# Optimization experiments

Measured on AMD Instinct MI355X. Metric: run time of the kernel, lower is better.

The kernel has to match this reference:

```python
import jax, jax.numpy as jnp
import numpy as np

N_ENTITY = 200000
N_RELATIONS = 32
DIM = 64
N_HOP = 2
N_MEMORY = 32
BATCH = 1024
KGE_WEIGHT = 0.01
L2_WEIGHT = 1e-7


def setup_inputs() -> dict:
    key = jax.random.key(0)
    ks = jax.random.split(key, 8)
    items = jax.random.randint(ks[0], (BATCH,), 0, N_ENTITY)
    labels = jax.random.uniform(ks[1], (BATCH,), dtype=jnp.float32)
    memories_h = jax.random.randint(ks[2], (N_HOP, BATCH, N_MEMORY), 0, N_ENTITY)
    memories_r = jax.random.randint(ks[3], (N_HOP, BATCH, N_MEMORY), 0, N_RELATIONS)
    memories_t = jax.random.randint(ks[4], (N_HOP, BATCH, N_MEMORY), 0, N_ENTITY)
    item_table = jax.random.normal(ks[5], (N_ENTITY, DIM), dtype=jnp.float32) * 0.1
    relation_table = jax.random.normal(ks[6], (N_RELATIONS, DIM * DIM), dtype=jnp.float32) * 0.1
    transform_W = jax.random.normal(ks[7], (DIM, DIM), dtype=jnp.float32) * 0.1
    return dict(items=items, labels=labels, memories_h=memories_h,
                memories_r=memories_r, memories_t=memories_t,
                item_table=item_table, relation_table=relation_table,
                transform_W=transform_W)


def _forward(items, labels, memories_h, memories_r, memories_t,
             item_table, relation_table, transform_W):
    v = item_table[items]  # [B, D]
    o_list = []
    kge_loss = jnp.float32(0.0)
    l2_loss = jnp.float32(0.0)
    for hop in range(N_HOP):
        h = item_table[memories_h[hop]]                                   # [B, M, D]
        R = relation_table[memories_r[hop]].reshape(-1, N_MEMORY, DIM, DIM)  # [B, M, D, D]
        t = item_table[memories_t[hop]]                                   # [B, M, D]
        # Rh = R @ h  -> [B, M, D]
        Rh = jnp.einsum('bmij,bmj->bmi', R, h)
        # attention probs over memory slots
        probs = jax.nn.softmax(jnp.einsum('bmi,bi->bm', Rh, v), axis=-1)  # [B, M]
        o = jnp.einsum('bmd,bm->bd', t, probs)                            # [B, D]
        # item_update_mode == 'plus_transform': v = W(v + o)
        v = (v + o) @ transform_W.T
        o_list.append(o)
        # KGE loss: sigmoid(h^T R t), mean over [B, M]
        hRt = jnp.einsum('bmi,bmij,bmj->bm', h, R, t)
        kge_loss = kge_loss + jnp.mean(jax.nn.sigmoid(hRt))
        l2_loss = l2_loss + jnp.sum(h * h) + jnp.sum(t * t) + jnp.sum(R * R)
    kge_loss = -KGE_WEIGHT * kge_loss
    l2_loss = L2_WEIGHT * l2_loss
    # predict with all hops
    y = o_list[-1]
    for i in range(N_HOP - 1):
        y = y + o_list[i]
    scores = jax.nn.sigmoid(jnp.sum(v * y, axis=1))  # [B]
    # BCE loss (torch clamps log at -100)
    logp = jnp.clip(jnp.log(scores), -100.0)
    lognp = jnp.clip(jnp.log(1.0 - scores), -100.0)
    base_loss = -jnp.mean(labels * logp + (1.0 - labels) * lognp)
    loss = base_loss + kge_loss + l2_loss
    return scores, loss, base_loss, kge_loss, l2_loss


def reference(items, labels, memories_h, memories_r, memories_t,
              item_table, relation_table, transform_W):
    return _forward(items, labels, memories_h, memories_r, memories_t,
                    item_table, relation_table, transform_W)
```

## Files before the change

kernel.cpp:

```cpp
#include <hip/hip_runtime.h>
#include <math.h>

#define N_ENTITY 200000
#define N_REL 32
#define DIM 64
#define N_HOP 2
#define N_MEM 32
#define BATCH 1024
#define PAIR_PER_HOP (BATCH * N_MEM)
#define N_PAIR (N_HOP * PAIR_PER_HOP)
#define CAP 3072
#define JBLK 32
#define WPB 4
#define NBLK_PAIRS (JBLK * N_REL * WPB)
#define TPAD 68

typedef __attribute__((ext_vector_type(8))) short short8;
typedef __attribute__((ext_vector_type(4))) float floatx4;

__device__ __forceinline__ float wave_reduce_sum(float v) {
    v += __shfl_xor(v, 1);
    v += __shfl_xor(v, 2);
    v += __shfl_xor(v, 4);
    v += __shfl_xor(v, 8);
    v += __shfl_xor(v, 16);
    v += __shfl_xor(v, 32);
    return v;
}

__device__ __forceinline__ unsigned short f2b(float x) {
    union { float f; unsigned u; } c; c.f = x;
    const unsigned r = (c.u + 0x7FFFu + ((c.u >> 16) & 1u)) >> 16;
    return (unsigned short)r;
}

__device__ __forceinline__ float b2f(short s) {
    union { unsigned u; float f; } c;
    c.u = ((unsigned)(unsigned short)s) << 16;
    return c.f;
}

__device__ __forceinline__ short8 pack8(const float4 a, const float4 b) {
    short8 s;
    s[0] = (short)f2b(a.x); s[1] = (short)f2b(a.y);
    s[2] = (short)f2b(a.z); s[3] = (short)f2b(a.w);
    s[4] = (short)f2b(b.x); s[5] = (short)f2b(b.y);
    s[6] = (short)f2b(b.z); s[7] = (short)f2b(b.w);
    return s;
}

__device__ __forceinline__ float sq4(const float4 a) {
    return a.x * a.x + a.y * a.y + a.z * a.z + a.w * a.w;
}

__device__ __forceinline__ float dot4(const float4 a, const float4 b) {
    return a.x * b.x + a.y * b.y + a.z * b.z + a.w * b.w;
}

__global__ __launch_bounds__(256) void ripple_bin(
    const int* __restrict__ mr,
    int* __restrict__ g_cnt,
    int* __restrict__ list)
{
    __shared__ int hist[N_REL];
    __shared__ int cur[N_REL];
    const int tid = (int)threadIdx.x;
    const int pbase = (int)blockIdx.x * 1024;

    if (tid < N_REL) hist[tid] = 0;
    __syncthreads();

    int rv[4];
    #pragma unroll
    for (int u = 0; u < 4; ++u) {
        rv[u] = mr[pbase + u * 256 + tid];
        atomicAdd(&hist[rv[u]], 1);
    }
    __syncthreads();
    if (tid < N_REL) cur[tid] = atomicAdd(&g_cnt[tid], hist[tid]);
    __syncthreads();
    #pragma unroll
    for (int u = 0; u < 4; ++u) {
        const int r = rv[u];
        const int pos = atomicAdd(&cur[r], 1);
        if (pos < CAP) list[r * CAP + pos] = pbase + u * 256 + tid;
    }
}

__global__ __launch_bounds__(256) void ripple_pairs(
    const int* __restrict__ items,
    const int* __restrict__ mh,
    const int* __restrict__ mt,
    const float* __restrict__ item_table,
    const float* __restrict__ rel_table,
    const int* __restrict__ g_cnt,
    const int* __restrict__ list,
    float* __restrict__ wsL,
    unsigned short* __restrict__ wsRh,
    float* __restrict__ ws_kge,
    float* __restrict__ ws_l2)
{
    __shared__ __align__(16) float sTr[WPB][16 * TPAD];
    __shared__ __align__(16) short8 sB[512];
    __shared__ float sRed[WPB];

    const int tid = (int)threadIdx.x;
    const int lane = tid & 63;
    const int w = tid >> 6;
    const int j = (int)blockIdx.x;
    const int r = (int)blockIdx.y;
    const int n = min(g_cnt[r], CAP);

    const int m16 = lane & 15;
    const int quad = lane >> 4;
    const int rb = r * CAP;
    const int wave_id = j * WPB + w;

    float* __restrict__ buf = &sTr[w][0];

    int tau = wave_id;
    int p = 0, hidx = 0, tidx = 0, iidx = 0;
    if (tau * 16 < n) {
        const int pos = min(tau * 16 + m16, n - 1);
        p = list[rb + pos];
        hidx = mh[p];
        tidx = mt[p];
        iidx = (p < PAIR_PER_HOP) ? items[p >> 5] : 0;
    }

    {
        const float* __restrict__ Rb = rel_table + (size_t)r * (DIM * DIM);
        float rsq = 0.f;
        #pragma unroll
        for (int u = 0; u < 2; ++u) {
            const int slot = tid + 256 * u;
            const int s = slot >> 8;
            const int tn = (slot >> 6) & 3;
            const int ls = slot & 63;
            const float* src = Rb + (size_t)(16 * tn + (ls & 15)) * DIM
                             + 32 * s + 8 * (ls >> 4);
            const float4 a = *(const float4*)src;
            const float4 b = *(const float4*)(src + 4);
            rsq += sq4(a) + sq4(b);
            sB[slot] = pack8(a, b);
        }
        rsq = wave_reduce_sum(rsq);
        if (lane == 0) sRed[w] = rsq;
    }
    __syncthreads();
    const float Rsum = sRed[0] + sRed[1] + sRed[2] + sRed[3];

    short8 Bf[2][4];
    #pragma unroll
    for (int s = 0; s < 2; ++s)
        #pragma unroll
        for (int tn = 0; tn < 4; ++tn)
            Bf[s][tn] = sB[s * 256 + tn * 64 + lane];

    float kge = 0.f;
    float l2ht = 0.f;
    int cnt = 0;

    for (; tau * 16 < n; tau += JBLK * WPB) {
        const int base = tau * 16;
        const bool mvalid = (base + m16) < n;
        const bool hop0 = p < PAIR_PER_HOP;

        const float* __restrict__ hp = item_table + (size_t)hidx * DIM + 8 * quad;
        const float* __restrict__ tp = item_table + (size_t)tidx * DIM + 8 * quad;
        const float4 h0a = *(const float4*)hp;
        const float4 h0b = *(const float4*)(hp + 4);
        const float4 h1a = *(const float4*)(hp + 32);
        const float4 h1b = *(const float4*)(hp + 36);
        const float4 t0a = *(const float4*)tp;
        const float4 t0b = *(const float4*)(tp + 4);
        const float4 t1a = *(const float4*)(tp + 32);
        const float4 t1b = *(const float4*)(tp + 36);

        float4 va0, va1, va2, va3;
        va0 = va1 = va2 = va3 = make_float4(0.f, 0.f, 0.f, 0.f);
        if (hop0) {
            const float* __restrict__ vp =
                item_table + (size_t)iidx * DIM + 16 * quad;
            va0 = *(const float4*)vp;
            va1 = *(const float4*)(vp + 4);
            va2 = *(const float4*)(vp + 8);
            va3 = *(const float4*)(vp + 12);
        }

        const int tau2 = tau + JBLK * WPB;
        int p2 = 0, h2 = 0, t2 = 0, i2 = 0;
        if (tau2 * 16 < n) {
            const int pos2 = min(tau2 * 16 + m16, n - 1);
            p2 = list[rb + pos2];
            h2 = mh[p2];
            t2 = mt[p2];
            i2 = (p2 < PAIR_PER_HOP) ? items[p2 >> 5] : 0;
        }

        if (mvalid) {
            l2ht += sq4(h0a) + sq4(h0b) + sq4(h1a) + sq4(h1b)
                  + sq4(t0a) + sq4(t0b) + sq4(t1a) + sq4(t1b);
        }

        const short8 Ah0 = pack8(h0a, h0b);
        const short8 Ah1 = pack8(h1a, h1b);
        const short8 At0 = pack8(t0a, t0b);
        const short8 At1 = pack8(t1a, t1b);

        floatx4 Ch[4], Ct[4];
        const floatx4 z4 = {0.f, 0.f, 0.f, 0.f};
        #pragma unroll
        for (int tn = 0; tn < 4; ++tn) {
            Ch[tn] = __builtin_amdgcn_mfma_f32_16x16x32_bf16(Ah0, Bf[0][tn], z4, 0, 0, 0);
            Ch[tn] = __builtin_amdgcn_mfma_f32_16x16x32_bf16(Ah1, Bf[1][tn], Ch[tn], 0, 0, 0);
            Ct[tn] = __builtin_amdgcn_mfma_f32_16x16x32_bf16(At0, Bf[0][tn], z4, 0, 0, 0);
            Ct[tn] = __builtin_amdgcn_mfma_f32_16x16x32_bf16(At1, Bf[1][tn], Ct[tn], 0, 0, 0);
        }

        #pragma unroll
        for (int tn = 0; tn < 4; ++tn) {
            const int col = m16 + 16 * tn;
            #pragma unroll
            for (int q = 0; q < 4; ++q)
                buf[(4 * quad + q) * TPAD + col] = Ct[tn][q];
        }
        const float* rowT = buf + m16 * TPAD;
        const float4 ct0 = *(const float4*)(rowT + 8 * quad);
        const float4 ct1 = *(const float4*)(rowT + 8 * quad + 4);
        const float4 ct2 = *(const float4*)(rowT + 32 + 8 * quad);
        const float4 ct3 = *(const float4*)(rowT + 32 + 8 * quad + 4);
        float hrt = dot4(h0a, ct0) + dot4(h0b, ct1) + dot4(h1a, ct2) + dot4(h1b, ct3);
        hrt += __shfl_xor(hrt, 16);
        hrt += __shfl_xor(hrt, 32);

        #pragma unroll
        for (int tn = 0; tn < 4; ++tn) {
            const int col = m16 + 16 * tn;
            #pragma unroll
            for (int q = 0; q < 4; ++q)
                buf[(4 * quad + q) * TPAD + col] = Ch[tn][q];
        }
        const float* rowC = buf + m16 * TPAD;
        const float4 c0 = *(const float4*)(rowC + 16 * quad);
        const float4 c1 = *(const float4*)(rowC + 16 * quad + 4);
        const float4 c2 = *(const float4*)(rowC + 16 * quad + 8);
        const float4 c3 = *(const float4*)(rowC + 16 * quad + 12);

        float lg = dot4(va0, c0) + dot4(va1, c1) + dot4(va2, c2) + dot4(va3, c3);
        lg += __shfl_xor(lg, 16);
        lg += __shfl_xor(lg, 32);

        if (quad == 0 && mvalid) {
            kge += 1.f / (1.f + expf(-hrt));
            if (hop0) wsL[p] = lg;
        }

        if (mvalid && !hop0) {
            unsigned short* __restrict__ dst =
                wsRh + (size_t)(p - PAIR_PER_HOP) * DIM + 16 * quad;
            *(short8*)dst = pack8(c0, c1);
            *(short8*)(dst + 8) = pack8(c2, c3);
        }

        cnt += min(16, n - base);
        p = p2; hidx = h2; tidx = t2; iidx = i2;
    }

    const float l2tot = wave_reduce_sum(l2ht) + (float)cnt * Rsum;
    const float kgetot = wave_reduce_sum(kge);
    if (lane == 0) {
        const int bid = (r * JBLK + j) * WPB + w;
        ws_kge[bid] = kgetot;
        ws_l2[bid] = l2tot;
    }
}

__global__ __launch_bounds__(256) void ripple_attn(
    const int* __restrict__ items,
    const float* __restrict__ labels,
    const int* __restrict__ mt,
    const float* __restrict__ item_table,
    const float* __restrict__ W,
    const float* __restrict__ wsL,
    const unsigned short* __restrict__ wsRh,
    float* __restrict__ out,
    float* __restrict__ ws_bce)
{
    __shared__ float sAtt[N_MEM];
    __shared__ __align__(16) float sO[4][DIM];
    __shared__ __align__(16) float sV[DIM];

    const int b = (int)blockIdx.x;
    const int tid = (int)threadIdx.x;
    const int lane = tid & 63;
    const int w = tid >> 6;

    const float v0 = item_table[(size_t)items[b] * DIM + lane];

    float l0 = 0.f;
    if (tid < N_MEM) l0 = wsL[b * N_MEM + tid];

    float treg[2][8];
    #pragma unroll
    for (int hop = 0; hop < 2; ++hop)
        #pragma unroll
        for (int q = 0; q < 8; ++q) {
            const int tidx = mt[hop * PAIR_PER_HOP + b * N_MEM + w * 8 + q];
            treg[hop][q] = item_table[(size_t)tidx * DIM + lane];
        }

    const int m1 = tid >> 3;
    const int d1 = (tid & 7) * 8;
    const short8 rv8 =
        *(const short8*)(wsRh + (size_t)(b * N_MEM + m1) * DIM + d1);

    const float lab = labels[b];

    if (tid < N_MEM) sAtt[tid] = l0;
    __syncthreads();

    float mx = -1e30f;
    #pragma unroll
    for (int m = 0; m < N_MEM; ++m) mx = fmaxf(mx, sAtt[m]);
    float se = 0.f;
    float e_loc[8];
    #pragma unroll
    for (int m = 0; m < N_MEM; ++m) {
        const float e = expf(sAtt[m] - mx);
        se += e;
        if ((m >> 3) == w) e_loc[m & 7] = e;
    }
    float inv = 1.f / se;

    float op = 0.f;
    #pragma unroll
    for (int q = 0; q < 8; ++q) op = fmaf(treg[0][q], e_loc[q] * inv, op);
    sO[w][lane] = op;
    __syncthreads();

    float y0 = 0.f, v1 = 0.f;
    if (w == 0) {
        const float o0 = sO[0][lane] + sO[1][lane] + sO[2][lane] + sO[3][lane];
        y0 = o0;
        sV[lane] = v0 + o0;
        const float4* __restrict__ Wrow = (const float4*)(W + (size_t)lane * DIM);
        float a0 = 0.f, a1 = 0.f, a2 = 0.f, a3 = 0.f;
        #pragma unroll
        for (int k = 0; k < 16; ++k) {
            const float4 w4 = Wrow[k];
            const float4 u4 = *(const float4*)&sV[k * 4];
            a0 = fmaf(w4.x, u4.x, a0);
            a1 = fmaf(w4.y, u4.y, a1);
            a2 = fmaf(w4.z, u4.z, a2);
            a3 = fmaf(w4.w, u4.w, a3);
        }
        v1 = (a0 + a1) + (a2 + a3);
        sV[lane] = v1;
    }
    __syncthreads();

    {
        float dp = 0.f;
        #pragma unroll
        for (int e = 0; e < 8; ++e) dp = fmaf(b2f(rv8[e]), sV[d1 + e], dp);
        dp += __shfl_xor(dp, 1);
        dp += __shfl_xor(dp, 2);
        dp += __shfl_xor(dp, 4);
        if ((tid & 7) == 0) sAtt[m1] = dp;
    }
    __syncthreads();

    mx = -1e30f;
    #pragma unroll
    for (int m = 0; m < N_MEM; ++m) mx = fmaxf(mx, sAtt[m]);
    se = 0.f;
    #pragma unroll
    for (int m = 0; m < N_MEM; ++m) {
        const float e = expf(sAtt[m] - mx);
        se += e;
        if ((m >> 3) == w) e_loc[m & 7] = e;
    }
    inv = 1.f / se;

    op = 0.f;
    #pragma unroll
    for (int q = 0; q < 8; ++q) op = fmaf(treg[1][q], e_loc[q] * inv, op);
    sO[w][lane] = op;
    __syncthreads();

    if (w != 0) return;

    const float o1 = sO[0][lane] + sO[1][lane] + sO[2][lane] + sO[3][lane];
    const float y = y0 + o1;
    sV[lane] = v1 + o1;
    const float4* __restrict__ Wrow = (const float4*)(W + (size_t)lane * DIM);
    float a0 = 0.f, a1 = 0.f, a2 = 0.f, a3 = 0.f;
    #pragma unroll
    for (int k = 0; k < 16; ++k) {
        const float4 w4 = Wrow[k];
        const float4 u4 = *(const float4*)&sV[k * 4];
        a0 = fmaf(w4.x, u4.x, a0);
        a1 = fmaf(w4.y, u4.y, a1);
        a2 = fmaf(w4.z, u4.z, a2);
        a3 = fmaf(w4.w, u4.w, a3);
    }
    const float v2 = (a0 + a1) + (a2 + a3);

    float s = wave_reduce_sum(v2 * y);
    s = 1.f / (1.f + expf(-s));
    if (lane == 0) {
        out[b] = s;
        const float logp = fmaxf(logf(s), -100.f);
        const float lognp = fmaxf(logf(1.f - s), -100.f);
        ws_bce[b] = lab * logp + (1.f - lab) * lognp;
    }
}

__global__ __launch_bounds__(256) void ripple_finalize(
    const float* __restrict__ ws_bce,
    const float* __restrict__ ws_kge,
    const float* __restrict__ ws_l2,
    float* __restrict__ out)
{
    __shared__ float sb[4], sk[4], sl[4];
    const int tid = (int)threadIdx.x;
    float bsum = 0.f, ksum = 0.f, lsum = 0.f;
    for (int i = tid; i < BATCH; i += 256) bsum += ws_bce[i];
    for (int i = tid; i < NBLK_PAIRS; i += 256) {
        ksum += ws_kge[i];
        lsum += ws_l2[i];
    }
    bsum = wave_reduce_sum(bsum);
    ksum = wave_reduce_sum(ksum);
    lsum = wave_reduce_sum(lsum);
    const int w = tid >> 6;
    if ((tid & 63) == 0) { sb[w] = bsum; sk[w] = ksum; sl[w] = lsum; }
    __syncthreads();
    if (tid == 0) {
        const float bs = sb[0] + sb[1] + sb[2] + sb[3];
        const float ks = sk[0] + sk[1] + sk[2] + sk[3];
        const float ls = sl[0] + sl[1] + sl[2] + sl[3];
        const float base_loss = -bs / (float)BATCH;
        const float kge_loss = -0.01f * (ks / (float)(BATCH * N_MEM));
        const float l2_loss = 1e-7f * ls;
        out[BATCH + 0] = base_loss + kge_loss + l2_loss;
        out[BATCH + 1] = base_loss;
        out[BATCH + 2] = kge_loss;
        out[BATCH + 3] = l2_loss;
    }
}

extern "C" void kernel_launch(void* const* d_in, const int* in_sizes, int n_in,
                              void* d_out, int out_size, void* d_ws, size_t ws_size,
                              hipStream_t stream) {
    const int* items        = (const int*)d_in[0];
    const float* labels     = (const float*)d_in[1];
    const int* mh           = (const int*)d_in[2];
    const int* mr           = (const int*)d_in[3];
    const int* mt           = (const int*)d_in[4];
    const float* item_table = (const float*)d_in[5];
    const float* rel_table  = (const float*)d_in[6];
    const float* W          = (const float*)d_in[7];
    float* out = (float*)d_out;

    float* ws = (float*)d_ws;
    float* wsL            = ws;
    unsigned short* wsRh  = (unsigned short*)(wsL + PAIR_PER_HOP);
    int*   list           = (int*)(wsRh + (size_t)PAIR_PER_HOP * DIM);
    int*   g_cnt          = list + N_REL * CAP;
    float* ws_bce         = (float*)(g_cnt + N_REL);
    float* ws_kge         = ws_bce + BATCH;
    float* ws_l2          = ws_kge + NBLK_PAIRS;

    hipMemsetAsync(g_cnt, 0, N_REL * sizeof(int), stream);
    ripple_bin<<<N_PAIR / 1024, 256, 0, stream>>>(mr, g_cnt, list);
    dim3 gpairs(JBLK, N_REL);
    ripple_pairs<<<gpairs, 256, 0, stream>>>(items, mh, mt, item_table, rel_table,
                                             g_cnt, list, wsL, wsRh, ws_kge, ws_l2);
    ripple_attn<<<BATCH, 256, 0, stream>>>(items, labels, mt, item_table, W,
                                           wsL, wsRh, out, ws_bce);
    ripple_finalize<<<1, 256, 0, stream>>>(ws_bce, ws_kge, ws_l2, out);
}
```

Baseline: 135.9 us.

## Fuse all phases into one cooperative persistent kernel with grid syncs

Merges the binning, pair, attention and finalize kernels into a single cooperative-launch kernel of 768 blocks that separates phases with grid.sync, removing the memset and several kernel launch gaps. Binning is made deterministic with a two-pass histogram and prefix offset instead of global atomics. The pair grid shrinks from 32 to 24 blocks per relation, and attention loops over the batch with a grid stride. A multi-kernel fallback runs if the cooperative launch fails. In exchange it adds grid-wide barrier cost, caps occupancy at 3 blocks per CU, and leaves fewer blocks to hide the gather latency in the pair phase.

```diff
diff --git a/kernel.cpp b/kernel.cpp
--- a/kernel.cpp
+++ b/kernel.cpp
@@ -1,4 +1,5 @@
 #include <hip/hip_runtime.h>
+#include <hip/hip_cooperative_groups.h>
 #include <math.h>
 
 #define N_ENTITY 200000
@@ -10,13 +11,31 @@
 #define PAIR_PER_HOP (BATCH * N_MEM)
 #define N_PAIR (N_HOP * PAIR_PER_HOP)
 #define CAP 3072
-#define JBLK 32
+#define NBLOCKS 768
+#define JBLK 24
 #define WPB 4
 #define NBLK_PAIRS (JBLK * N_REL * WPB)
 #define TPAD 68
+#define BINB 64
+
+namespace cg = cooperative_groups;
 
 typedef __attribute__((ext_vector_type(8))) short short8;
 typedef __attribute__((ext_vector_type(4))) float floatx4;
+
+struct SmemA { int hist[N_REL]; int cur[N_REL]; };
+struct __align__(16) SmemB {
+    float sTr[WPB][16 * TPAD];
+    short8 sB[512];
+    float sRed[WPB];
+};
+struct __align__(16) SmemC {
+    float sAtt[N_MEM];
+    float sO[4][DIM];
+    float sV[DIM];
+};
+struct SmemD { float sb[4], sk[4], sl[4]; };
+union __align__(16) Smem { SmemA a; SmemB b; SmemC c; SmemD d; };
 
 __device__ __forceinline__ float wave_reduce_sum(float v) {
     v += __shfl_xor(v, 1);
@@ -57,37 +76,43 @@
     return a.x * b.x + a.y * b.y + a.z * b.z + a.w * b.w;
 }
 
-__global__ __launch_bounds__(256) void ripple_bin(
-    const int* __restrict__ mr,
-    int* __restrict__ g_cnt,
-    int* __restrict__ list)
-{
-    __shared__ int hist[N_REL];
-    __shared__ int cur[N_REL];
-    const int tid = (int)threadIdx.x;
-    const int pbase = (int)blockIdx.x * 1024;
-
-    if (tid < N_REL) hist[tid] = 0;
-    __syncthreads();
-
-    int rv[4];
+__device__ __forceinline__ void phaseA1(const int bid, const int tid,
+                                        const int* __restrict__ mr,
+                                        int* __restrict__ g_hist, SmemA& sa) {
+    const int pbase = bid * 1024;
+    if (tid < N_REL) sa.hist[tid] = 0;
+    __syncthreads();
+    #pragma unroll
+    for (int u = 0; u < 4; ++u)
+        atomicAdd(&sa.hist[mr[pbase + u * 256 + tid]], 1);
+    __syncthreads();
+    if (tid < N_REL) g_hist[bid * N_REL + tid] = sa.hist[tid];
+}
+
+__device__ __forceinline__ void phaseA2(const int bid, const int tid,
+                                        const int* __restrict__ mr,
+                                        const int* __restrict__ g_hist,
+                                        int* __restrict__ list,
+                                        int* __restrict__ g_cnt, SmemA& sa) {
+    if (tid < N_REL) {
+        int off = 0;
+        for (int b = 0; b < bid; ++b) off += g_hist[b * N_REL + tid];
+        sa.cur[tid] = off;
+        if (bid == BINB - 1) g_cnt[tid] = off + g_hist[bid * N_REL + tid];
+    }
+    __syncthreads();
+    const int pbase = bid * 1024;
     #pragma unroll
     for (int u = 0; u < 4; ++u) {
-        rv[u] = mr[pbase + u * 256 + tid];
-        atomicAdd(&hist[rv[u]], 1);
-    }
-    __syncthreads();
-    if (tid < N_REL) cur[tid] = atomicAdd(&g_cnt[tid], hist[tid]);
-    __syncthreads();
-    #pragma unroll
-    for (int u = 0; u < 4; ++u) {
-        const int r = rv[u];
-        const int pos = atomicAdd(&cur[r], 1);
-        if (pos < CAP) list[r * CAP + pos] = pbase + u * 256 + tid;
-    }
-}
-
-__global__ __launch_bounds__(256) void ripple_pairs(
+        const int idx = pbase + u * 256 + tid;
+        const int r = mr[idx];
+        const int pos = atomicAdd(&sa.cur[r], 1);
+        if (pos < CAP) list[r * CAP + pos] = idx;
+    }
+}
+
+__device__ __forceinline__ void phaseB(
+    const int bid, const int tid,
     const int* __restrict__ items,
     const int* __restrict__ mh,
     const int* __restrict__ mt,
@@ -98,17 +123,13 @@
     float* __restrict__ wsL,
     unsigned short* __restrict__ wsRh,
     float* __restrict__ ws_kge,
-    float* __restrict__ ws_l2)
+    float* __restrict__ ws_l2,
+    SmemB& sb)
 {
-    __shared__ __align__(16) float sTr[WPB][16 * TPAD];
-    __shared__ __align__(16) short8 sB[512];
-    __shared__ float sRed[WPB];
-
-    const int tid = (int)threadIdx.x;
     const int lane = tid & 63;
     const int w = tid >> 6;
-    const int j = (int)blockIdx.x;
-    const int r = (int)blockIdx.y;
+    const int j = bid % JBLK;
+    const int r = bid / JBLK;
     const int n = min(g_cnt[r], CAP);
 
     const int m16 = lane & 15;
@@ -116,7 +137,7 @@
     const int rb = r * CAP;
     const int wave_id = j * WPB + w;
 
-    float* __restrict__ buf = &sTr[w][0];
+    float* buf = &sb.sTr[w][0];
 
     int tau = wave_id;
     int p = 0, hidx = 0, tidx = 0, iidx = 0;
@@ -142,20 +163,20 @@
             const float4 a = *(const float4*)src;
             const float4 b = *(const float4*)(src + 4);
             rsq += sq4(a) + sq4(b);
-            sB[slot] = pack8(a, b);
+            sb.sB[slot] = pack8(a, b);
         }
         rsq = wave_reduce_sum(rsq);
-        if (lane == 0) sRed[w] = rsq;
-    }
-    __syncthreads();
-    const float Rsum = sRed[0] + sRed[1] + sRed[2] + sRed[3];
+        if (lane == 0) sb.sRed[w] = rsq;
+    }
+    __syncthreads();
+    const float Rsum = sb.sRed[0] + sb.sRed[1] + sb.sRed[2] + sb.sRed[3];
 
     short8 Bf[2][4];
     #pragma unroll
     for (int s = 0; s < 2; ++s)
         #pragma unroll
         for (int tn = 0; tn < 4; ++tn)
-            Bf[s][tn] = sB[s * 256 + tn * 64 + lane];
+            Bf[s][tn] = sb.sB[s * 256 + tn * 64 + lane];
 
     float kge = 0.f;
     float l2ht = 0.f;
@@ -270,13 +291,14 @@
     const float l2tot = wave_reduce_sum(l2ht) + (float)cnt * Rsum;
     const float kgetot = wave_reduce_sum(kge);
     if (lane == 0) {
-        const int bid = (r * JBLK + j) * WPB + w;
-        ws_kge[bid] = kgetot;
-        ws_l2[bid] = l2tot;
-    }
-}
-
-__global__ __launch_bounds__(256) void ripple_attn(
+        const int slot = (r * JBLK + j) * WPB + w;
+        ws_kge[slot] = kgetot;
+        ws_l2[slot] = l2tot;
+    }
+}
+
+__device__ __forceinline__ void phaseC_one(
+    const int b, const int tid,
     const int* __restrict__ items,
     const float* __restrict__ labels,
     const int* __restrict__ mt,
@@ -285,14 +307,9 @@
     const float* __restrict__ wsL,
     const unsigned short* __restrict__ wsRh,
     float* __restrict__ out,
-    float* __restrict__ ws_bce)
+    float* __restrict__ ws_bce,
+    SmemC& sc)
 {
-    __shared__ float sAtt[N_MEM];
-    __shared__ __align__(16) float sO[4][DIM];
-    __shared__ __align__(16) float sV[DIM];
-
-    const int b = (int)blockIdx.x;
-    const int tid = (int)threadIdx.x;
     const int lane = tid & 63;
     const int w = tid >> 6;
 
@@ -317,17 +334,17 @@
 
     const float lab = labels[b];
 
-    if (tid < N_MEM) sAtt[tid] = l0;
+    if (tid < N_MEM) sc.sAtt[tid] = l0;
     __syncthreads();
 
     float mx = -1e30f;
     #pragma unroll
-    for (int m = 0; m < N_MEM; ++m) mx = fmaxf(mx, sAtt[m]);
+    for (int m = 0; m < N_MEM; ++m) mx = fmaxf(mx, sc.sAtt[m]);
     float se = 0.f;
     float e_loc[8];
     #pragma unroll
     for (int m = 0; m < N_MEM; ++m) {
-        const float e = expf(sAtt[m] - mx);
+        const float e = expf(sc.sAtt[m] - mx);
         se += e;
         if ((m >> 3) == w) e_loc[m & 7] = e;
     }
@@ -336,48 +353,48 @@
     float op = 0.f;
     #pragma unroll
     for (int q = 0; q < 8; ++q) op = fmaf(treg[0][q], e_loc[q] * inv, op);
-    sO[w][lane] = op;
+    sc.sO[w][lane] = op;
     __syncthreads();
 
     float y0 = 0.f, v1 = 0.f;
     if (w == 0) {
-        const float o0 = sO[0][lane] + sO[1][lane] + sO[2][lane] + sO[3][lane];
+        const float o0 = sc.sO[0][lane] + sc.sO[1][lane] + sc.sO[2][lane] + sc.sO[3][lane];
         y0 = o0;
-        sV[lane] = v0 + o0;
+        sc.sV[lane] = v0 + o0;
         const float4* __restrict__ Wrow = (const float4*)(W + (size_t)lane * DIM);
         float a0 = 0.f, a1 = 0.f, a2 = 0.f, a3 = 0.f;
         #pragma unroll
         for (int k = 0; k < 16; ++k) {
             const float4 w4 = Wrow[k];
-            const float4 u4 = *(const float4*)&sV[k * 4];
+            const float4 u4 = *(const float4*)&sc.sV[k * 4];
             a0 = fmaf(w4.x, u4.x, a0);
             a1 = fmaf(w4.y, u4.y, a1);
             a2 = fmaf(w4.z, u4.z, a2);
             a3 = fmaf(w4.w, u4.w, a3);
         }
         v1 = (a0 + a1) + (a2 + a3);
-        sV[lane] = v1;
+        sc.sV[lane] = v1;
     }
     __syncthreads();
 
     {
         float dp = 0.f;
         #pragma unroll
-        for (int e = 0; e < 8; ++e) dp = fmaf(b2f(rv8[e]), sV[d1 + e], dp);
+        for (int e = 0; e < 8; ++e) dp = fmaf(b2f(rv8[e]), sc.sV[d1 + e], dp);
         dp += __shfl_xor(dp, 1);
         dp += __shfl_xor(dp, 2);
         dp += __shfl_xor(dp, 4);
-        if ((tid & 7) == 0) sAtt[m1] = dp;
+        if ((tid & 7) == 0) sc.sAtt[m1] = dp;
     }
     __syncthreads();
 
     mx = -1e30f;
     #pragma unroll
-    for (int m = 0; m < N_MEM; ++m) mx = fmaxf(mx, sAtt[m]);
+    for (int m = 0; m < N_MEM; ++m) mx = fmaxf(mx, sc.sAtt[m]);
     se = 0.f;
     #pragma unroll
     for (int m = 0; m < N_MEM; ++m) {
-        const float e = expf(sAtt[m] - mx);
+        const float e = expf(sc.sAtt[m] - mx);
         se += e;
         if ((m >> 3) == w) e_loc[m & 7] = e;
     }
@@ -386,45 +403,57 @@
     op = 0.f;
     #pragma unroll
     for (int q = 0; q < 8; ++q) op = fmaf(treg[1][q], e_loc[q] * inv, op);
-    sO[w][lane] = op;
-    __syncthreads();
-
-    if (w != 0) return;
-
-    const float o1 = sO[0][lane] + sO[1][lane] + sO[2][lane] + sO[3][lane];
-    const float y = y0 + o1;
-    sV[lane] = v1 + o1;
-    const float4* __restrict__ Wrow = (const float4*)(W + (size_t)lane * DIM);
-    float a0 = 0.f, a1 = 0.f, a2 = 0.f, a3 = 0.f;
-    #pragma unroll
-    for (int k = 0; k < 16; ++k) {
-        const float4 w4 = Wrow[k];
-        const float4 u4 = *(const float4*)&sV[k * 4];
-        a0 = fmaf(w4.x, u4.x, a0);
-        a1 = fmaf(w4.y, u4.y, a1);
-        a2 = fmaf(w4.z, u4.z, a2);
-        a3 = fmaf(w4.w, u4.w, a3);
-    }
-    const float v2 = (a0 + a1) + (a2 + a3);
-
-    float s = wave_reduce_sum(v2 * y);
-    s = 1.f / (1.f + expf(-s));
-    if (lane == 0) {
-        out[b] = s;
-        const float logp = fmaxf(logf(s), -100.f);
-        const float lognp = fmaxf(logf(1.f - s), -100.f);
-        ws_bce[b] = lab * logp + (1.f - lab) * lognp;
-    }
-}
-
-__global__ __launch_bounds__(256) void ripple_finalize(
+    sc.sO[w][lane] = op;
+    __syncthreads();
+
+    if (w == 0) {
+        const float o1 = sc.sO[0][lane] + sc.sO[1][lane] + sc.sO[2][lane] + sc.sO[3][lane];
+        const float y = y0 + o1;
+        sc.sV[lane] = v1 + o1;
+        const float4* __restrict__ Wrow = (const float4*)(W + (size_t)lane * DIM);
+        float a0 = 0.f, a1 = 0.f, a2 = 0.f, a3 = 0.f;
+        #pragma unroll
+        for (int k = 0; k < 16; ++k) {
+            const float4 w4 = Wrow[k];
+            const float4 u4 = *(const float4*)&sc.sV[k * 4];
+            a0 = fmaf(w4.x, u4.x, a0);
+            a1 = fmaf(w4.y, u4.y, a1);
+            a2 = fmaf(w4.z, u4.z, a2);
+            a3 = fmaf(w4.w, u4.w, a3);
+        }
+        const float v2 = (a0 + a1) + (a2 + a3);
+
+        float s = wave_reduce_sum(v2 * y);
+        s = 1.f / (1.f + expf(-s));
+        if (lane == 0) {
+            out[b] = s;
+            const float logp = fmaxf(logf(s), -100.f);
+            const float lognp = fmaxf(logf(1.f - s), -100.f);
+            ws_bce[b] = lab * logp + (1.f - lab) * lognp;
+        }
+    }
+}
+
+__device__ __forceinline__ void phaseC_all(
+    const int bid, const int tid,
+    const int* __restrict__ items, const float* __restrict__ labels,
+    const int* __restrict__ mt, const float* __restrict__ item_table,
+    const float* __restrict__ W, const float* __restrict__ wsL,
+    const unsigned short* __restrict__ wsRh,
+    float* __restrict__ out, float* __restrict__ ws_bce, SmemC& sc)
+{
+    for (int b = bid; b < BATCH; b += NBLOCKS)
+        phaseC_one(b, tid, items, labels, mt, item_table, W, wsL, wsRh,
+                   out, ws_bce, sc);
+}
+
+__device__ __forceinline__ void phaseD(
+    const int tid,
     const float* __restrict__ ws_bce,
     const float* __restrict__ ws_kge,
     const float* __restrict__ ws_l2,
-    float* __restrict__ out)
+    float* __restrict__ out, SmemD& sd)
 {
-    __shared__ float sb[4], sk[4], sl[4];
-    const int tid = (int)threadIdx.x;
     float bsum = 0.f, ksum = 0.f, lsum = 0.f;
     for (int i = tid; i < BATCH; i += 256) bsum += ws_bce[i];
     for (int i = tid; i < NBLK_PAIRS; i += 256) {
@@ -435,12 +464,12 @@
     ksum = wave_reduce_sum(ksum);
     lsum = wave_reduce_sum(lsum);
     const int w = tid >> 6;
-    if ((tid & 63) == 0) { sb[w] = bsum; sk[w] = ksum; sl[w] = lsum; }
+    if ((tid & 63) == 0) { sd.sb[w] = bsum; sd.sk[w] = ksum; sd.sl[w] = lsum; }
     __syncthreads();
     if (tid == 0) {
-        const float bs = sb[0] + sb[1] + sb[2] + sb[3];
-        const float ks = sk[0] + sk[1] + sk[2] + sk[3];
-        const float ls = sl[0] + sl[1] + sl[2] + sl[3];
+        const float bs = sd.sb[0] + sd.sb[1] + sd.sb[2] + sd.sb[3];
+        const float ks = sd.sk[0] + sd.sk[1] + sd.sk[2] + sd.sk[3];
+        const float ls = sd.sl[0] + sd.sl[1] + sd.sl[2] + sd.sl[3];
         const float base_loss = -bs / (float)BATCH;
         const float kge_loss = -0.01f * (ks / (float)(BATCH * N_MEM));
         const float l2_loss = 1e-7f * ls;
@@ -449,6 +478,78 @@
         out[BATCH + 2] = kge_loss;
         out[BATCH + 3] = l2_loss;
     }
+}
+
+__global__ __launch_bounds__(256, 3) void ripple_fused(
+    const int* __restrict__ items, const float* __restrict__ labels,
+    const int* __restrict__ mh, const int* __restrict__ mr,
+    const int* __restrict__ mt,
+    const float* __restrict__ item_table, const float* __restrict__ rel_table,
+    const float* __restrict__ W,
+    float* __restrict__ wsL, unsigned short* __restrict__ wsRh,
+    int* __restrict__ list, int* __restrict__ g_hist, int* __restrict__ g_cnt,
+    float* __restrict__ ws_bce, float* __restrict__ ws_kge,
+    float* __restrict__ ws_l2, float* __restrict__ out)
+{
+    __shared__ Smem sm;
+    const int bid = (int)blockIdx.x;
+    const int tid = (int)threadIdx.x;
+    cg::grid_group grid = cg::this_grid();
+
+    if (bid < BINB) phaseA1(bid, tid, mr, g_hist, sm.a);
+    grid.sync();
+    if (bid < BINB) phaseA2(bid, tid, mr, g_hist, list, g_cnt, sm.a);
+    grid.sync();
+    phaseB(bid, tid, items, mh, mt, item_table, rel_table, g_cnt, list,
+           wsL, wsRh, ws_kge, ws_l2, sm.b);
+    grid.sync();
+    phaseC_all(bid, tid, items, labels, mt, item_table, W, wsL, wsRh,
+               out, ws_bce, sm.c);
+    grid.sync();
+    if (bid == 0) phaseD(tid, ws_bce, ws_kge, ws_l2, out, sm.d);
+}
+
+__global__ __launch_bounds__(256) void k_bin1(
+    const int* __restrict__ mr, int* __restrict__ g_hist) {
+    __shared__ Smem sm;
+    phaseA1((int)blockIdx.x, (int)threadIdx.x, mr, g_hist, sm.a);
+}
+
+__global__ __launch_bounds__(256) void k_bin2(
+    const int* __restrict__ mr, const int* __restrict__ g_hist,
+    int* __restrict__ list, int* __restrict__ g_cnt) {
+    __shared__ Smem sm;
+    phaseA2((int)blockIdx.x, (int)threadIdx.x, mr, g_hist, list, g_cnt, sm.a);
+}
+
+__global__ __launch_bounds__(256) void k_pairs(
+    const int* __restrict__ items, const int* __restrict__ mh,
+    const int* __restrict__ mt, const float* __restrict__ item_table,
+    const float* __restrict__ rel_table, const int* __restrict__ g_cnt,
+    const int* __restrict__ list, float* __restrict__ wsL,
+    unsigned short* __restrict__ wsRh, float* __restrict__ ws_kge,
+    float* __restrict__ ws_l2) {
+    __shared__ Smem sm;
+    phaseB((int)blockIdx.x, (int)threadIdx.x, items, mh, mt, item_table,
+           rel_table, g_cnt, list, wsL, wsRh, ws_kge, ws_l2, sm.b);
+}
+
+__global__ __launch_bounds__(256) void k_attn(
+    const int* __restrict__ items, const float* __restrict__ labels,
+    const int* __restrict__ mt, const float* __restrict__ item_table,
+    const float* __restrict__ W, const float* __restrict__ wsL,
+    const unsigned short* __restrict__ wsRh, float* __restrict__ out,
+    float* __restrict__ ws_bce) {
+    __shared__ Smem sm;
+    phaseC_all((int)blockIdx.x, (int)threadIdx.x, items, labels, mt,
+               item_table, W, wsL, wsRh, out, ws_bce, sm.c);
+}
+
+__global__ __launch_bounds__(256) void k_fin(
+    const float* __restrict__ ws_bce, const float* __restrict__ ws_kge,
+    const float* __restrict__ ws_l2, float* __restrict__ out) {
+    __shared__ Smem sm;
+    phaseD((int)threadIdx.x, ws_bce, ws_kge, ws_l2, out, sm.d);
 }
 
 extern "C" void kernel_launch(void* const* d_in, const int* in_sizes, int n_in,
@@ -468,17 +569,29 @@
     float* wsL            = ws;
     unsigned short* wsRh  = (unsigned short*)(wsL + PAIR_PER_HOP);
     int*   list           = (int*)(wsRh + (size_t)PAIR_PER_HOP * DIM);
-    int*   g_cnt          = list + N_REL * CAP;
+    int*   g_hist         = list + N_REL * CAP;
+    int*   g_cnt          = g_hist + BINB * N_REL;
     float* ws_bce         = (float*)(g_cnt + N_REL);
     float* ws_kge         = ws_bce + BATCH;
     float* ws_l2          = ws_kge + NBLK_PAIRS;
 
-    hipMemsetAsync(g_cnt, 0, N_REL * sizeof(int), stream);
-    ripple_bin<<<N_PAIR / 1024, 256, 0, stream>>>(mr, g_cnt, list);
-    dim3 gpairs(JBLK, N_REL);
-    ripple_pairs<<<gpairs, 256, 0, stream>>>(items, mh, mt, item_table, rel_table,
-                                             g_cnt, list, wsL, wsRh, ws_kge, ws_l2);
-    ripple_attn<<<BATCH, 256, 0, stream>>>(items, labels, mt, item_table, W,
-                                           wsL, wsRh, out, ws_bce);
-    ripple_finalize<<<1, 256, 0, stream>>>(ws_bce, ws_kge, ws_l2, out);
-}
+    void* args[] = {
+        (void*)&items, (void*)&labels, (void*)&mh, (void*)&mr, (void*)&mt,
+        (void*)&item_table, (void*)&rel_table, (void*)&W,
+        (void*)&wsL, (void*)&wsRh, (void*)&list, (void*)&g_hist, (void*)&g_cnt,
+        (void*)&ws_bce, (void*)&ws_kge, (void*)&ws_l2, (void*)&out };
+
+    hipError_t err = hipLaunchCooperativeKernel(
+        (const void*)ripple_fused, dim3(NBLOCKS), dim3(256), args, 0, stream);
+    if (err != hipSuccess) {
+        (void)hipGetLastError();
+        k_bin1<<<BINB, 256, 0, stream>>>(mr, g_hist);
+        k_bin2<<<BINB, 256, 0, stream>>>(mr, g_hist, list, g_cnt);
+        k_pairs<<<NBLOCKS, 256, 0, stream>>>(items, mh, mt, item_table,
+                                             rel_table, g_cnt, list, wsL, wsRh,
+                                             ws_kge, ws_l2);
+        k_attn<<<NBLOCKS, 256, 0, stream>>>(items, labels, mt, item_table, W,
+                                            wsL, wsRh, out, ws_bce);
+        k_fin<<<1, 256, 0, stream>>>(ws_bce, ws_kge, ws_l2, out);
+    }
+}
```

New measurement: 463.7 us. 241% more time.

## Process one batch row per wavefront in attention kernel, removing block syncs

Applied to the files above, without the earlier changes.

The attention kernel now gives each wavefront its own batch element, four per block, instead of spreading one element over a 256-thread block. Softmax, the weighted sums and the Rh·v dot products use wave shuffles and a per-wave shared slice, so all __syncthreads are gone and idle waves no longer wait during the transform step. Each lane now holds 64 gathered tail values in registers, which raises register pressure and may reduce occupancy. The grid shrinks to BATCH/4 blocks.

```diff
diff --git a/kernel.cpp b/kernel.cpp
--- a/kernel.cpp
+++ b/kernel.cpp
@@ -287,125 +287,112 @@
     float* __restrict__ out,
     float* __restrict__ ws_bce)
 {
-    __shared__ float sAtt[N_MEM];
-    __shared__ __align__(16) float sO[4][DIM];
-    __shared__ __align__(16) float sV[DIM];
-
-    const int b = (int)blockIdx.x;
+    __shared__ __align__(16) float sV[4][DIM];
+
     const int tid = (int)threadIdx.x;
     const int lane = tid & 63;
     const int w = tid >> 6;
+    const int b = (int)blockIdx.x * 4 + w;
 
     const float v0 = item_table[(size_t)items[b] * DIM + lane];
 
-    float l0 = 0.f;
-    if (tid < N_MEM) l0 = wsL[b * N_MEM + tid];
-
-    float treg[2][8];
-    #pragma unroll
-    for (int hop = 0; hop < 2; ++hop)
-        #pragma unroll
-        for (int q = 0; q < 8; ++q) {
-            const int tidx = mt[hop * PAIR_PER_HOP + b * N_MEM + w * 8 + q];
-            treg[hop][q] = item_table[(size_t)tidx * DIM + lane];
-        }
-
-    const int m1 = tid >> 3;
-    const int d1 = (tid & 7) * 8;
-    const short8 rv8 =
-        *(const short8*)(wsRh + (size_t)(b * N_MEM + m1) * DIM + d1);
-
     const float lab = labels[b];
 
-    if (tid < N_MEM) sAtt[tid] = l0;
-    __syncthreads();
-
-    float mx = -1e30f;
-    #pragma unroll
-    for (int m = 0; m < N_MEM; ++m) mx = fmaxf(mx, sAtt[m]);
-    float se = 0.f;
-    float e_loc[8];
-    #pragma unroll
-    for (int m = 0; m < N_MEM; ++m) {
-        const float e = expf(sAtt[m] - mx);
-        se += e;
-        if ((m >> 3) == w) e_loc[m & 7] = e;
-    }
-    float inv = 1.f / se;
-
-    float op = 0.f;
-    #pragma unroll
-    for (int q = 0; q < 8; ++q) op = fmaf(treg[0][q], e_loc[q] * inv, op);
-    sO[w][lane] = op;
-    __syncthreads();
-
-    float y0 = 0.f, v1 = 0.f;
-    if (w == 0) {
-        const float o0 = sO[0][lane] + sO[1][lane] + sO[2][lane] + sO[3][lane];
-        y0 = o0;
-        sV[lane] = v0 + o0;
-        const float4* __restrict__ Wrow = (const float4*)(W + (size_t)lane * DIM);
+    float l0 = (lane < N_MEM) ? wsL[b * N_MEM + lane] : -1e30f;
+
+    const int myidx = mt[(lane >> 5) * PAIR_PER_HOP + b * N_MEM + (lane & 31)];
+
+    float treg[64];
+    #pragma unroll
+    for (int m = 0; m < 64; ++m) {
+        const int idx = __shfl(myidx, m);
+        treg[m] = item_table[(size_t)idx * DIM + lane];
+    }
+
+    const int m1 = lane >> 1;
+    const int d1 = (lane & 1) * 32;
+    short8 rv[4];
+    #pragma unroll
+    for (int e = 0; e < 4; ++e)
+        rv[e] = *(const short8*)(wsRh + (size_t)(b * N_MEM + m1) * DIM + d1 + 8 * e);
+
+    const float4* __restrict__ Wrow = (const float4*)(W + (size_t)lane * DIM);
+
+    float mx = l0;
+    #pragma unroll
+    for (int d = 16; d >= 1; d >>= 1) mx = fmaxf(mx, __shfl_xor(mx, d));
+    const float e0 = expf(l0 - mx);
+    float se = (lane < N_MEM) ? e0 : 0.f;
+    #pragma unroll
+    for (int d = 16; d >= 1; d >>= 1) se += __shfl_xor(se, d);
+    const float pe0 = e0 / se;
+
+    float o0 = 0.f;
+    #pragma unroll
+    for (int m = 0; m < N_MEM; ++m)
+        o0 = fmaf(treg[m], __shfl(pe0, m), o0);
+
+    sV[w][lane] = v0 + o0;
+    float v1;
+    {
         float a0 = 0.f, a1 = 0.f, a2 = 0.f, a3 = 0.f;
         #pragma unroll
         for (int k = 0; k < 16; ++k) {
             const float4 w4 = Wrow[k];
-            const float4 u4 = *(const float4*)&sV[k * 4];
+            const float4 u4 = *(const float4*)&sV[w][k * 4];
             a0 = fmaf(w4.x, u4.x, a0);
             a1 = fmaf(w4.y, u4.y, a1);
             a2 = fmaf(w4.z, u4.z, a2);
             a3 = fmaf(w4.w, u4.w, a3);
         }
         v1 = (a0 + a1) + (a2 + a3);
-        sV[lane] = v1;
-    }
-    __syncthreads();
-
+    }
+
+    sV[w][lane] = v1;
+    float dp = 0.f;
+    #pragma unroll
+    for (int e = 0; e < 4; ++e) {
+        const float4 va = *(const float4*)&sV[w][d1 + 8 * e];
+        const float4 vb = *(const float4*)&sV[w][d1 + 8 * e + 4];
+        dp += b2f(rv[e][0]) * va.x + b2f(rv[e][1]) * va.y
+            + b2f(rv[e][2]) * va.z + b2f(rv[e][3]) * va.w
+            + b2f(rv[e][4]) * vb.x + b2f(rv[e][5]) * vb.y
+            + b2f(rv[e][6]) * vb.z + b2f(rv[e][7]) * vb.w;
+    }
+    dp += __shfl_xor(dp, 1);
+    const float a1v = __shfl(dp, (lane & 31) * 2);
+
+    float av = (lane < N_MEM) ? a1v : -1e30f;
+    mx = av;
+    #pragma unroll
+    for (int d = 16; d >= 1; d >>= 1) mx = fmaxf(mx, __shfl_xor(mx, d));
+    const float e1 = expf(av - mx);
+    se = (lane < N_MEM) ? e1 : 0.f;
+    #pragma unroll
+    for (int d = 16; d >= 1; d >>= 1) se += __shfl_xor(se, d);
+    const float pe1 = e1 / se;
+
+    float o1 = 0.f;
+    #pragma unroll
+    for (int m = 0; m < N_MEM; ++m)
+        o1 = fmaf(treg[N_MEM + m], __shfl(pe1, m), o1);
+
+    const float y = o0 + o1;
+    sV[w][lane] = v1 + o1;
+    float v2;
     {
-        float dp = 0.f;
-        #pragma unroll
-        for (int e = 0; e < 8; ++e) dp = fmaf(b2f(rv8[e]), sV[d1 + e], dp);
-        dp += __shfl_xor(dp, 1);
-        dp += __shfl_xor(dp, 2);
-        dp += __shfl_xor(dp, 4);
-        if ((tid & 7) == 0) sAtt[m1] = dp;
-    }
-    __syncthreads();
-
-    mx = -1e30f;
-    #pragma unroll
-    for (int m = 0; m < N_MEM; ++m) mx = fmaxf(mx, sAtt[m]);
-    se = 0.f;
-    #pragma unroll
-    for (int m = 0; m < N_MEM; ++m) {
-        const float e = expf(sAtt[m] - mx);
-        se += e;
-        if ((m >> 3) == w) e_loc[m & 7] = e;
-    }
-    inv = 1.f / se;
-
-    op = 0.f;
-    #pragma unroll
-    for (int q = 0; q < 8; ++q) op = fmaf(treg[1][q], e_loc[q] * inv, op);
-    sO[w][lane] = op;
-    __syncthreads();
-
-    if (w != 0) return;
-
-    const float o1 = sO[0][lane] + sO[1][lane] + sO[2][lane] + sO[3][lane];
-    const float y = y0 + o1;
-    sV[lane] = v1 + o1;
-    const float4* __restrict__ Wrow = (const float4*)(W + (size_t)lane * DIM);
-    float a0 = 0.f, a1 = 0.f, a2 = 0.f, a3 = 0.f;
-    #pragma unroll
-    for (int k = 0; k < 16; ++k) {
-        const float4 w4 = Wrow[k];
-        const float4 u4 = *(const float4*)&sV[k * 4];
-        a0 = fmaf(w4.x, u4.x, a0);
-        a1 = fmaf(w4.y, u4.y, a1);
-        a2 = fmaf(w4.z, u4.z, a2);
-        a3 = fmaf(w4.w, u4.w, a3);
-    }
-    const float v2 = (a0 + a1) + (a2 + a3);
+        float a0 = 0.f, a1_ = 0.f, a2 = 0.f, a3 = 0.f;
+        #pragma unroll
+        for (int k = 0; k < 16; ++k) {
+            const float4 w4 = Wrow[k];
+            const float4 u4 = *(const float4*)&sV[w][k * 4];
+            a0 = fmaf(w4.x, u4.x, a0);
+            a1_ = fmaf(w4.y, u4.y, a1_);
+            a2 = fmaf(w4.z, u4.z, a2);
+            a3 = fmaf(w4.w, u4.w, a3);
+        }
+        v2 = (a0 + a1_) + (a2 + a3);
+    }
 
     float s = wave_reduce_sum(v2 * y);
     s = 1.f / (1.f + expf(-s));
@@ -478,7 +465,7 @@
     dim3 gpairs(JBLK, N_REL);
     ripple_pairs<<<gpairs, 256, 0, stream>>>(items, mh, mt, item_table, rel_table,
                                              g_cnt, list, wsL, wsRh, ws_kge, ws_l2);
-    ripple_attn<<<BATCH, 256, 0, stream>>>(items, labels, mt, item_table, W,
-                                           wsL, wsRh, out, ws_bce);
+    ripple_attn<<<BATCH / 4, 256, 0, stream>>>(items, labels, mt, item_table, W,
+                                               wsL, wsRh, out, ws_bce);
     ripple_finalize<<<1, 256, 0, stream>>>(ws_bce, ws_kge, ws_l2, out);
 }
```

Result: faster. 132.4 us (-2.5%).
